# Optimization experiments

Hardware: AMD Instinct MI355X
Metric: run time of the kernel (lower is better)

The kernel has to match this reference:

```python
import jax, jax.numpy as jnp
import numpy as np
import math

NUM_HEADS = 16


def setup_inputs() -> dict:
    key = jax.random.key(0)
    ks = jax.random.split(key, 5)
    L, B, E = 2048, 2, 1024
    scale = 1.0 / math.sqrt(E)
    return {
        "query": jax.random.normal(ks[0], (L, B, E), jnp.float32),
        "key": jax.random.normal(ks[1], (L, B, E), jnp.float32),
        "value": jax.random.normal(ks[2], (L, B, E), jnp.float32),
        "in_proj_weight": jax.random.normal(ks[3], (3 * E, E), jnp.float32) * scale,
        "in_proj_bias": jnp.zeros((3 * E,), jnp.float32),
        "out_w": jax.random.normal(ks[4], (E, E), jnp.float32) * scale,
        "out_b": jnp.zeros((E,), jnp.float32),
    }


def reference(query, key, value, in_proj_weight, in_proj_bias, out_w, out_b):
    L, Bz, E = query.shape
    S = key.shape[0]
    H = NUM_HEADS
    hd = E // H
    # in-projection: chunk packed weight into q/k/v parts (same math as torch chunk)
    w_q, w_k, w_v = jnp.split(in_proj_weight, 3, axis=0)
    b_q, b_k, b_v = jnp.split(in_proj_bias, 3, axis=0)
    q = query @ w_q.T + b_q            # (L, B, E)
    k = key @ w_k.T + b_k              # (S, B, E)
    v = value @ w_v.T + b_v            # (S, B, E)
    # (L, B*H, hd) -> (B*H, L, hd)
    q = q.reshape(L, Bz * H, hd).transpose(1, 0, 2) / math.sqrt(hd)
    k = k.reshape(S, Bz * H, hd).transpose(1, 0, 2)
    v = v.reshape(S, Bz * H, hd).transpose(1, 0, 2)
    # sigmoid attention (non-softmax), full (B*H, L, S) matrix as in original
    attn = jax.nn.sigmoid(jnp.einsum("bld,bsd->bls", q, k))
    denom = attn.sum(axis=-1, keepdims=True) + 1e-4
    out = jnp.einsum("bls,bsd->bld", attn / denom, v)  # (B*H, L, hd)
    out = out.transpose(1, 0, 2).reshape(L, Bz, E)
    out = out @ out_w.T + out_b
    avg_weights = attn.reshape(Bz, H, L, S).sum(axis=1) / H
    return out, avg_weights
```

## Files before the change

### kernel.cpp

```cpp
#include <hip/hip_runtime.h>
#include <stdint.h>


#define L_SEQ 2048
#define NBATCH 2
#define EMB 1024
#define NHEAD 16
#define HD 64
#define MROWS 4096

typedef __bf16 bf16x8 __attribute__((ext_vector_type(8)));
typedef float f32x4 __attribute__((ext_vector_type(4)));

#define WAITVM(N) asm volatile("s_waitcnt vmcnt(" #N ")" ::: "memory")
#define WAITLG() asm volatile("s_waitcnt lgkmcnt(0)" ::: "memory")
#define SBAR()                                  \
  do {                                          \
    asm volatile("" ::: "memory");              \
    __builtin_amdgcn_s_barrier();               \
    asm volatile("" ::: "memory");              \
  } while (0)

#if __has_builtin(__builtin_amdgcn_exp2f)
#define EXP2F(x) __builtin_amdgcn_exp2f(x)
#else
#define EXP2F(x) exp2f(x)
#endif

__device__ __forceinline__ unsigned short f2bf(float f) {
  union { float f; uint32_t u; } v; v.f = f;
  uint32_t u = v.u;
  u += 0x7fffu + ((u >> 16) & 1u);
  return (unsigned short)(u >> 16);
}

__device__ __forceinline__ unsigned short f2bf_fast(float f) {
  union { float f; uint32_t u; } v; v.f = f;
  return (unsigned short)((v.u + 0x8000u) >> 16);
}

__device__ __forceinline__ void gl_lds16(const void* gptr, void* ldsptr) {
  const uint32_t* g = reinterpret_cast<const uint32_t*>(gptr);
  auto* l = reinterpret_cast<__attribute__((address_space(3))) uint32_t*>(
      reinterpret_cast<uintptr_t>(ldsptr));
  __builtin_amdgcn_global_load_lds(g, l, 16, 0, 0);
}

__device__ __forceinline__ f32x4 mfma16(bf16x8 a, bf16x8 b, f32x4 c) {
  return __builtin_amdgcn_mfma_f32_16x16x32_bf16(a, b, c, 0, 0, 0);
}

__device__ __forceinline__ float fast_sigmoid2(float st) {
  float e = EXP2F(st);
  return __builtin_amdgcn_rcpf(1.0f + e);
}

__global__ __launch_bounds__(256) void k_convert(
    const float* __restrict__ qin, const float* __restrict__ kin,
    const float* __restrict__ vin, const float* __restrict__ win,
    const float* __restrict__ wo,
    unsigned short* __restrict__ Xq, unsigned short* __restrict__ Xk,
    unsigned short* __restrict__ Xv, unsigned short* __restrict__ Wb,
    unsigned short* __restrict__ Wob) {
  const int row = blockIdx.x;
  const int t = threadIdx.x;
  const float* src;
  unsigned short* dst;
  int srow;
  size_t drow;
  if (row < 3 * MROWS) {
    const int which = row >> 12;
    const int m = row & (MROWS - 1);
    const int b = m >> 11, l = m & (L_SEQ - 1);
    srow = l * NBATCH + b;
    drow = (size_t)m;
    src = which == 0 ? qin : (which == 1 ? kin : vin);
    dst = which == 0 ? Xq : (which == 1 ? Xk : Xv);
  } else if (row < 3 * MROWS + 3072) {
    srow = row - 3 * MROWS; drow = (size_t)srow; src = win; dst = Wb;
  } else {
    srow = row - (3 * MROWS + 3072); drow = (size_t)srow; src = wo; dst = Wob;
  }
  const float4 vv = *(const float4*)(src + (size_t)srow * EMB + t * 4);
  ushort4 o;
  o.x = f2bf(vv.x); o.y = f2bf(vv.y); o.z = f2bf(vv.z); o.w = f2bf(vv.w);
  *(ushort4*)(dst + drow * EMB + t * 4) = o;
}

__device__ __forceinline__ void gemm_issue(
    const unsigned short* __restrict__ A, const unsigned short* __restrict__ Bm,
    int m0, int n0, int k0, unsigned short* sA, unsigned short* sB) {
  const int tid = threadIdx.x;
  const int wave = tid >> 6;
  const int lane = tid & 63;
  const int srow = lane >> 2;
  const int scol = lane & 3;
  for (int i = 0; i < 2; ++i) {
    const int p = wave * 2 + i;
    const int r = p * 16 + srow;
    const int c = scol ^ ((r >> 1) & 3);
    gl_lds16(A + (size_t)(m0 + r) * EMB + k0 + c * 8, sA + p * 512);
    gl_lds16(Bm + (size_t)(n0 + r) * EMB + k0 + c * 8, sB + p * 512);
  }
}

__device__ __forceinline__ void gemm_core(
    const unsigned short* __restrict__ A, const unsigned short* __restrict__ Bm,
    int m0, int n0, unsigned short* sA, unsigned short* sB, f32x4 acc[4][4]) {
  const int tid = threadIdx.x;
  const int wave = tid >> 6;
  const int lane = tid & 63;
  const int quad = lane >> 4;
  const int l16 = lane & 15;
  const int wm = (wave >> 1) * 64;
  const int wn = (wave & 1) * 64;
  const int NSTEP = EMB / 32;

  for (int mi = 0; mi < 4; ++mi)
    for (int ni = 0; ni < 4; ++ni)
      acc[mi][ni] = (f32x4){0.f, 0.f, 0.f, 0.f};

  gemm_issue(A, Bm, m0, n0, 0, sA, sB);
  gemm_issue(A, Bm, m0, n0, 32, sA + 4096, sB + 4096);

  int cur = 0;
  for (int step = 0; step < NSTEP; ++step) {
    if (step < NSTEP - 1) { WAITVM(4); } else { WAITVM(0); }
    SBAR();
    if (step + 2 < NSTEP) {
      int nxt = cur + 2; if (nxt >= 3) nxt -= 3;
      gemm_issue(A, Bm, m0, n0, (step + 2) * 32, sA + nxt * 4096,
                 sB + nxt * 4096);
    }
    const unsigned short* cA = sA + cur * 4096;
    const unsigned short* cB = sB + cur * 4096;
    bf16x8 af[4], bfr[4];
    for (int mi = 0; mi < 4; ++mi) {
      const int r = wm + mi * 16 + l16;
      const int cp = quad ^ ((r >> 1) & 3);
      af[mi] = *(const bf16x8*)(cA + r * 32 + cp * 8);
    }
    for (int ni = 0; ni < 4; ++ni) {
      const int r = wn + ni * 16 + l16;
      const int cp = quad ^ ((r >> 1) & 3);
      bfr[ni] = *(const bf16x8*)(cB + r * 32 + cp * 8);
    }
    for (int mi = 0; mi < 4; ++mi)
      for (int ni = 0; ni < 4; ++ni)
        acc[mi][ni] = mfma16(af[mi], bfr[ni], acc[mi][ni]);
    cur = cur == 2 ? 0 : cur + 1;
  }
}

__global__ __launch_bounds__(256) void k_inproj(
    const unsigned short* __restrict__ Xq, const unsigned short* __restrict__ Xk,
    const unsigned short* __restrict__ Xv, const unsigned short* __restrict__ Wb,
    const float* __restrict__ bias,
    unsigned short* __restrict__ qb, unsigned short* __restrict__ kb,
    unsigned short* __restrict__ vb) {
  __shared__ __attribute__((aligned(16))) unsigned short sA[3 * 128 * 32];
  __shared__ __attribute__((aligned(16))) unsigned short sB[3 * 128 * 32];
  const int bid = blockIdx.x;
  const int tile = (bid & 7) * 96 + (bid >> 3);
  const int z = tile >> 8;
  const int rem = tile & 255;
  const int m0 = (rem >> 3) * 128;
  const int n0 = (rem & 7) * 128;
  const unsigned short* A = z == 0 ? Xq : (z == 1 ? Xk : Xv);
  f32x4 acc[4][4];
  gemm_core(A, Wb + (size_t)z * EMB * EMB, m0, n0, sA, sB, acc);

  const int tid = threadIdx.x, wave = tid >> 6, lane = tid & 63;
  const int quad = lane >> 4, l16 = lane & 15;
  const int wm = (wave >> 1) * 64, wn = (wave & 1) * 64;
  const float scale = (z == 0) ? -0.18033688011112042f : 1.0f;
  unsigned short* dst01 = (z == 0) ? qb : kb;
  for (int ni = 0; ni < 4; ++ni) {
    const int n = n0 + wn + ni * 16 + l16;
    const float bv = bias[z * EMB + n];
    const int h = n >> 6, d = n & 63;
    for (int mi = 0; mi < 4; ++mi) {
      for (int r = 0; r < 4; ++r) {
        const int m = m0 + wm + mi * 16 + quad * 4 + r;
        const int b = m >> 11, l = m & (L_SEQ - 1);
        const unsigned short o = f2bf((acc[mi][ni][r] + bv) * scale);
        if (z == 2)
          vb[((size_t)(b * NHEAD + h) * HD + d) * L_SEQ + l] = o;
        else
          dst01[((size_t)(b * NHEAD + h) * L_SEQ + l) * HD + d] = o;
      }
    }
  }
}

__global__ __launch_bounds__(512) void k_attn(
    const unsigned short* __restrict__ qb, const unsigned short* __restrict__ kb,
    const unsigned short* __restrict__ vb, unsigned short* __restrict__ oh) {
  __shared__ __attribute__((aligned(16))) unsigned short sK[2][64 * 64];
  __shared__ __attribute__((aligned(16))) unsigned short sV[2][64 * 64];
  __shared__ __attribute__((aligned(16))) unsigned short sP[128 * 72];

  const int bh = blockIdx.x;
  const int b = bh >> 4, h = bh & 15;
  const int l0 = blockIdx.y * 128;
  const unsigned short* qg = qb + ((size_t)bh * L_SEQ + l0) * HD;
  const unsigned short* kg = kb + (size_t)bh * L_SEQ * HD;
  const unsigned short* vg = vb + (size_t)bh * HD * L_SEQ;

  const int tid = threadIdx.x, wave = tid >> 6, lane = tid & 63;
  const int quad = lane >> 4, l16 = lane & 15;
  const int sr8 = lane >> 3, sc8 = lane & 7;
  const int W = wave * 16;

  bf16x8 qf0, qf1;
  {
    const unsigned short* qrow = qg + (size_t)(W + l16) * HD + quad * 8;
    qf0 = *(const bf16x8*)(qrow);
    qf1 = *(const bf16x8*)(qrow + 32);
  }

  if (wave < 4) {
    for (int i = 0; i < 2; ++i) {
      const int p = wave * 2 + i;
      const int r = p * 8 + sr8;
      const int c = sc8 ^ (r & 7);
      gl_lds16(kg + (size_t)r * HD + c * 8, sK[0] + p * 512);
    }
  } else {
    for (int i = 0; i < 2; ++i) {
      const int p = (wave - 4) * 2 + i;
      const int r = p * 8 + sr8;
      const int c = sc8 ^ (r & 7);
      gl_lds16(vg + (size_t)r * L_SEQ + c * 8, sV[0] + p * 512);
    }
  }

  f32x4 oacc[4];
  for (int ni = 0; ni < 4; ++ni) oacc[ni] = (f32x4){0.f, 0.f, 0.f, 0.f};
  f32x4 dacc = (f32x4){0.f, 0.f, 0.f, 0.f};

  bf16x8 ones;
  for (int j = 0; j < 8; ++j) ones[j] = (__bf16)1.0f;

  const int NS = L_SEQ / 64;
  for (int it = 0; it < NS; ++it) {
    const int cur = it & 1;
    WAITVM(0);
    SBAR();
    if (it + 1 < NS) {
      const int s0n = (it + 1) * 64;
      if (wave < 4) {
        for (int i = 0; i < 2; ++i) {
          const int p = wave * 2 + i;
          const int r = p * 8 + sr8;
          const int c = sc8 ^ (r & 7);
          gl_lds16(kg + (size_t)(s0n + r) * HD + c * 8, sK[cur ^ 1] + p * 512);
        }
      } else {
        for (int i = 0; i < 2; ++i) {
          const int p = (wave - 4) * 2 + i;
          const int r = p * 8 + sr8;
          const int c = sc8 ^ (r & 7);
          gl_lds16(vg + (size_t)r * L_SEQ + s0n + c * 8, sV[cur ^ 1] + p * 512);
        }
      }
    }

    f32x4 st[4];
    for (int smi = 0; smi < 4; ++smi) st[smi] = (f32x4){0.f, 0.f, 0.f, 0.f};
    {
      for (int smi = 0; smi < 4; ++smi) {
        const int r = smi * 16 + l16;
        const int c = quad ^ (r & 7);
        bf16x8 a = *(const bf16x8*)(sK[cur] + r * 64 + c * 8);
        st[smi] = mfma16(a, qf0, st[smi]);
      }
    }
    {
      for (int smi = 0; smi < 4; ++smi) {
        const int r = smi * 16 + l16;
        const int c = (4 + quad) ^ (r & 7);
        bf16x8 a = *(const bf16x8*)(sK[cur] + r * 64 + c * 8);
        st[smi] = mfma16(a, qf1, st[smi]);
      }
    }

    for (int smi = 0; smi < 4; ++smi) {
      uint32_t u[4];
      for (int r = 0; r < 4; ++r) {
        union { float f; uint32_t i; } cv;
        cv.f = fast_sigmoid2(st[smi][r]);
        u[r] = cv.i + 0x8000u;
      }
      uint2 pk;
      pk.x = __builtin_amdgcn_perm(u[1], u[0], 0x07060302u);
      pk.y = __builtin_amdgcn_perm(u[3], u[2], 0x07060302u);
      *(uint2*)(sP + (size_t)(W + l16) * 72 + smi * 16 + quad * 4) = pk;
    }
    WAITLG();

    const int lr = W + l16;
    for (int kk = 0; kk < 64; kk += 32) {
      bf16x8 ap = *(const bf16x8*)(sP + (size_t)lr * 72 + kk + quad * 8);
      for (int ni = 0; ni < 4; ++ni) {
        const int rd = ni * 16 + l16;
        const int c = ((kk >> 3) + quad) ^ (rd & 7);
        bf16x8 bv4 = *(const bf16x8*)(sV[cur] + rd * 64 + c * 8);
        oacc[ni] = mfma16(ap, bv4, oacc[ni]);
      }
      dacc = mfma16(ap, ones, dacc);
    }
  }

  for (int r = 0; r < 4; ++r) {
    const int lrow = l0 + wave * 16 + quad * 4 + r;
    const float rden = __builtin_amdgcn_rcpf(dacc[r] + 1e-4f);
    unsigned short* dst = oh + ((size_t)(b * L_SEQ + lrow)) * EMB + h * HD;
    for (int ni = 0; ni < 4; ++ni)
      dst[ni * 16 + l16] = f2bf_fast(oacc[ni][r] * rden);
  }
}

__global__ __launch_bounds__(512) void k_avg(
    const unsigned short* __restrict__ qb, const unsigned short* __restrict__ kb,
    float* __restrict__ avg) {
  __shared__ __attribute__((aligned(16))) unsigned short sQ[2][128 * 64];
  __shared__ __attribute__((aligned(16))) unsigned short sK[2][128 * 64];
  const int ss0 = blockIdx.x * 128, l0 = blockIdx.y * 128, b = blockIdx.z;
  const int tid = threadIdx.x, wave = tid >> 6, lane = tid & 63;
  const int quad = lane >> 4, l16 = lane & 15;
  const int wm = (wave & 1) * 64, wn = (wave >> 1) * 32;
  const int sr8 = lane >> 3, sc8 = lane & 7;

  f32x4 av[4][2];
  for (int mi = 0; mi < 4; ++mi)
    for (int ni = 0; ni < 2; ++ni) av[mi][ni] = (f32x4){0.f, 0.f, 0.f, 0.f};

  auto stage = [&](int hh, int buf) {
    const unsigned short* qg = qb + ((size_t)(b * NHEAD + hh) * L_SEQ + l0) * HD;
    const unsigned short* kg = kb + ((size_t)(b * NHEAD + hh) * L_SEQ + ss0) * HD;
    for (int i = 0; i < 2; ++i) {
      const int p = wave * 2 + i;
      const int r = p * 8 + sr8;
      const int c = sc8 ^ (r & 7);
      gl_lds16(qg + (size_t)r * HD + c * 8, sQ[buf] + p * 512);
      gl_lds16(kg + (size_t)r * HD + c * 8, sK[buf] + p * 512);
    }
  };

  stage(0, 0);

  for (int h = 0; h < NHEAD; ++h) {
    const int cur = h & 1;
    WAITVM(0);
    SBAR();
    if (h + 1 < NHEAD) stage(h + 1, cur ^ 1);

    f32x4 scr[4][2];
    for (int mi = 0; mi < 4; ++mi)
      for (int ni = 0; ni < 2; ++ni) scr[mi][ni] = (f32x4){0.f, 0.f, 0.f, 0.f};
    for (int kk = 0; kk < HD; kk += 32) {
      bf16x8 a[4], bb[2];
      for (int mi = 0; mi < 4; ++mi) {
        const int r = wm + mi * 16 + l16;
        const int c = ((kk >> 3) + quad) ^ (r & 7);
        a[mi] = *(const bf16x8*)(sQ[cur] + r * 64 + c * 8);
      }
      for (int ni = 0; ni < 2; ++ni) {
        const int r = wn + ni * 16 + l16;
        const int c = ((kk >> 3) + quad) ^ (r & 7);
        bb[ni] = *(const bf16x8*)(sK[cur] + r * 64 + c * 8);
      }
      for (int mi = 0; mi < 4; ++mi)
        for (int ni = 0; ni < 2; ++ni)
          scr[mi][ni] = mfma16(a[mi], bb[ni], scr[mi][ni]);
    }
    for (int mi = 0; mi < 4; ++mi)
      for (int ni = 0; ni < 2; ++ni)
        for (int r = 0; r < 4; ++r)
          av[mi][ni][r] += fast_sigmoid2(scr[mi][ni][r]);
  }

  for (int mi = 0; mi < 4; ++mi) {
    for (int r = 0; r < 4; ++r) {
      const int l = l0 + wm + mi * 16 + quad * 4 + r;
      float* dst = avg + ((size_t)b * L_SEQ + l) * L_SEQ + ss0 + wn;
      for (int ni = 0; ni < 2; ++ni)
        dst[ni * 16 + l16] = av[mi][ni][r] * 0.0625f;
    }
  }
}

__global__ __launch_bounds__(256) void k_outproj(
    const unsigned short* __restrict__ OH, const unsigned short* __restrict__ Wob,
    const float* __restrict__ ob, float* __restrict__ out) {
  __shared__ __attribute__((aligned(16))) unsigned short sA[3 * 128 * 32];
  __shared__ __attribute__((aligned(16))) unsigned short sB[3 * 128 * 32];
  const int bid = blockIdx.x;
  const int tile = (bid & 7) * 32 + (bid >> 3);
  const int m0 = (tile >> 3) * 128;
  const int n0 = (tile & 7) * 128;
  f32x4 acc[4][4];
  gemm_core(OH, Wob, m0, n0, sA, sB, acc);

  const int tid = threadIdx.x, wave = tid >> 6, lane = tid & 63;
  const int quad = lane >> 4, l16 = lane & 15;
  const int wm = (wave >> 1) * 64, wn = (wave & 1) * 64;
  for (int ni = 0; ni < 4; ++ni) {
    const int n = n0 + wn + ni * 16 + l16;
    const float bv = ob[n];
    for (int mi = 0; mi < 4; ++mi) {
      for (int r = 0; r < 4; ++r) {
        const int m = m0 + wm + mi * 16 + quad * 4 + r;
        const int b = m >> 11, l = m & (L_SEQ - 1);
        out[((size_t)l * NBATCH + b) * EMB + n] = acc[mi][ni][r] + bv;
      }
    }
  }
}

extern "C" void kernel_launch(void* const* d_in, const int* in_sizes, int n_in,
                              void* d_out, int out_size, void* d_ws, size_t ws_size,
                              hipStream_t stream) {
  (void)in_sizes; (void)n_in; (void)out_size;
  const float* qin = (const float*)d_in[0];
  const float* kin = (const float*)d_in[1];
  const float* vin = (const float*)d_in[2];
  const float* w   = (const float*)d_in[3];
  const float* bias = (const float*)d_in[4];
  const float* wo  = (const float*)d_in[5];
  const float* ob  = (const float*)d_in[6];
  float* out = (float*)d_out;

  unsigned short* Xq  = (unsigned short*)d_ws;
  unsigned short* Xk  = Xq + (size_t)MROWS * EMB;
  unsigned short* Xv  = Xk + (size_t)MROWS * EMB;
  unsigned short* Wb  = Xv + (size_t)MROWS * EMB;
  unsigned short* Wob = Wb + (size_t)3 * EMB * EMB;
  unsigned short* qbuf = Wob + (size_t)EMB * EMB;
  unsigned short* kbuf = qbuf + (size_t)MROWS * EMB;
  unsigned short* vbuf = kbuf + (size_t)MROWS * EMB;
  unsigned short* ohb  = vbuf + (size_t)MROWS * EMB;
  const size_t need = ((size_t)MROWS * EMB * 7 + (size_t)4 * EMB * EMB) * 2;
  if (ws_size < need) return;

  k_convert<<<16384, 256, 0, stream>>>(qin, kin, vin, w, wo, Xq, Xk, Xv, Wb, Wob);
  k_inproj<<<768, 256, 0, stream>>>(Xq, Xk, Xv, Wb, bias, qbuf, kbuf, vbuf);
  k_attn<<<dim3(32, 16), 512, 0, stream>>>(qbuf, kbuf, vbuf, ohb);
  k_avg<<<dim3(16, 16, 2), 512, 0, stream>>>(qbuf, kbuf, out + (size_t)MROWS * EMB);
  k_outproj<<<256, 256, 0, stream>>>(ohb, Wob, ob, out);
}
```

Before: 270.4 us.

## Merge attention and averaged-weights kernels into one launch with shared LDS

Combines the attention kernel and the head-averaged sigmoid weights kernel into a single kernel with 1024 blocks. Block ids below 512 run attention and the rest compute the averaged weights, with both roles using one 64 KB shared buffer. The aim is to let the two independent workloads run on the GPU at the same time and to save one kernel launch and the tail gap between kernels. In exchange, every block reserves the larger LDS footprint, which may limit how many attention blocks fit on a CU, and register use becomes the maximum of the two paths.

```diff
diff --git a/kernel.cpp b/kernel.cpp
--- a/kernel.cpp
+++ b/kernel.cpp
@@ -193,200 +193,206 @@
   }
 }
 
-__global__ __launch_bounds__(512) void k_attn(
+__global__ __launch_bounds__(512) void k_attn_avg(
     const unsigned short* __restrict__ qb, const unsigned short* __restrict__ kb,
-    const unsigned short* __restrict__ vb, unsigned short* __restrict__ oh) {
-  __shared__ __attribute__((aligned(16))) unsigned short sK[2][64 * 64];
-  __shared__ __attribute__((aligned(16))) unsigned short sV[2][64 * 64];
-  __shared__ __attribute__((aligned(16))) unsigned short sP[128 * 72];
-
-  const int bh = blockIdx.x;
-  const int b = bh >> 4, h = bh & 15;
-  const int l0 = blockIdx.y * 128;
-  const unsigned short* qg = qb + ((size_t)bh * L_SEQ + l0) * HD;
-  const unsigned short* kg = kb + (size_t)bh * L_SEQ * HD;
-  const unsigned short* vg = vb + (size_t)bh * HD * L_SEQ;
-
+    const unsigned short* __restrict__ vb, unsigned short* __restrict__ oh,
+    float* __restrict__ avg) {
+  __shared__ __attribute__((aligned(16))) unsigned short smem[32768];
+
+  const int aid = blockIdx.x;
   const int tid = threadIdx.x, wave = tid >> 6, lane = tid & 63;
   const int quad = lane >> 4, l16 = lane & 15;
   const int sr8 = lane >> 3, sc8 = lane & 7;
-  const int W = wave * 16;
-
-  bf16x8 qf0, qf1;
-  {
-    const unsigned short* qrow = qg + (size_t)(W + l16) * HD + quad * 8;
-    qf0 = *(const bf16x8*)(qrow);
-    qf1 = *(const bf16x8*)(qrow + 32);
-  }
-
-  if (wave < 4) {
-    for (int i = 0; i < 2; ++i) {
-      const int p = wave * 2 + i;
-      const int r = p * 8 + sr8;
-      const int c = sc8 ^ (r & 7);
-      gl_lds16(kg + (size_t)r * HD + c * 8, sK[0] + p * 512);
+
+  if (aid < 512) {
+    unsigned short (*sK)[64 * 64] = (unsigned short (*)[64 * 64])(smem);
+    unsigned short (*sV)[64 * 64] = (unsigned short (*)[64 * 64])(smem + 8192);
+    unsigned short* sP = smem + 16384;
+
+    const int bh = aid & 31;
+    const int b = bh >> 4, h = bh & 15;
+    const int l0 = (aid >> 5) * 128;
+    const unsigned short* qg = qb + ((size_t)bh * L_SEQ + l0) * HD;
+    const unsigned short* kg = kb + (size_t)bh * L_SEQ * HD;
+    const unsigned short* vg = vb + (size_t)bh * HD * L_SEQ;
+
+    const int W = wave * 16;
+
+    bf16x8 qf0, qf1;
+    {
+      const unsigned short* qrow = qg + (size_t)(W + l16) * HD + quad * 8;
+      qf0 = *(const bf16x8*)(qrow);
+      qf1 = *(const bf16x8*)(qrow + 32);
+    }
+
+    if (wave < 4) {
+      for (int i = 0; i < 2; ++i) {
+        const int p = wave * 2 + i;
+        const int r = p * 8 + sr8;
+        const int c = sc8 ^ (r & 7);
+        gl_lds16(kg + (size_t)r * HD + c * 8, sK[0] + p * 512);
+      }
+    } else {
+      for (int i = 0; i < 2; ++i) {
+        const int p = (wave - 4) * 2 + i;
+        const int r = p * 8 + sr8;
+        const int c = sc8 ^ (r & 7);
+        gl_lds16(vg + (size_t)r * L_SEQ + c * 8, sV[0] + p * 512);
+      }
+    }
+
+    f32x4 oacc[4];
+    for (int ni = 0; ni < 4; ++ni) oacc[ni] = (f32x4){0.f, 0.f, 0.f, 0.f};
+    f32x4 dacc = (f32x4){0.f, 0.f, 0.f, 0.f};
+
+    bf16x8 ones;
+    for (int j = 0; j < 8; ++j) ones[j] = (__bf16)1.0f;
+
+    const int NS = L_SEQ / 64;
+    for (int it = 0; it < NS; ++it) {
+      const int cur = it & 1;
+      WAITVM(0);
+      SBAR();
+      if (it + 1 < NS) {
+        const int s0n = (it + 1) * 64;
+        if (wave < 4) {
+          for (int i = 0; i < 2; ++i) {
+            const int p = wave * 2 + i;
+            const int r = p * 8 + sr8;
+            const int c = sc8 ^ (r & 7);
+            gl_lds16(kg + (size_t)(s0n + r) * HD + c * 8, sK[cur ^ 1] + p * 512);
+          }
+        } else {
+          for (int i = 0; i < 2; ++i) {
+            const int p = (wave - 4) * 2 + i;
+            const int r = p * 8 + sr8;
+            const int c = sc8 ^ (r & 7);
+            gl_lds16(vg + (size_t)r * L_SEQ + s0n + c * 8, sV[cur ^ 1] + p * 512);
+          }
+        }
+      }
+
+      f32x4 st[4];
+      for (int smi = 0; smi < 4; ++smi) st[smi] = (f32x4){0.f, 0.f, 0.f, 0.f};
+      {
+        for (int smi = 0; smi < 4; ++smi) {
+          const int r = smi * 16 + l16;
+          const int c = quad ^ (r & 7);
+          bf16x8 a = *(const bf16x8*)(sK[cur] + r * 64 + c * 8);
+          st[smi] = mfma16(a, qf0, st[smi]);
+        }
+      }
+      {
+        for (int smi = 0; smi < 4; ++smi) {
+          const int r = smi * 16 + l16;
+          const int c = (4 + quad) ^ (r & 7);
+          bf16x8 a = *(const bf16x8*)(sK[cur] + r * 64 + c * 8);
+          st[smi] = mfma16(a, qf1, st[smi]);
+        }
+      }
+
+      for (int smi = 0; smi < 4; ++smi) {
+        uint32_t u[4];
+        for (int r = 0; r < 4; ++r) {
+          union { float f; uint32_t i; } cv;
+          cv.f = fast_sigmoid2(st[smi][r]);
+          u[r] = cv.i + 0x8000u;
+        }
+        uint2 pk;
+        pk.x = __builtin_amdgcn_perm(u[1], u[0], 0x07060302u);
+        pk.y = __builtin_amdgcn_perm(u[3], u[2], 0x07060302u);
+        *(uint2*)(sP + (size_t)(W + l16) * 72 + smi * 16 + quad * 4) = pk;
+      }
+      WAITLG();
+
+      const int lr = W + l16;
+      for (int kk = 0; kk < 64; kk += 32) {
+        bf16x8 ap = *(const bf16x8*)(sP + (size_t)lr * 72 + kk + quad * 8);
+        for (int ni = 0; ni < 4; ++ni) {
+          const int rd = ni * 16 + l16;
+          const int c = ((kk >> 3) + quad) ^ (rd & 7);
+          bf16x8 bv4 = *(const bf16x8*)(sV[cur] + rd * 64 + c * 8);
+          oacc[ni] = mfma16(ap, bv4, oacc[ni]);
+        }
+        dacc = mfma16(ap, ones, dacc);
+      }
+    }
+
+    for (int r = 0; r < 4; ++r) {
+      const int lrow = l0 + wave * 16 + quad * 4 + r;
+      const float rden = __builtin_amdgcn_rcpf(dacc[r] + 1e-4f);
+      unsigned short* dst = oh + ((size_t)(b * L_SEQ + lrow)) * EMB + h * HD;
+      for (int ni = 0; ni < 4; ++ni)
+        dst[ni * 16 + l16] = f2bf_fast(oacc[ni][r] * rden);
     }
   } else {
-    for (int i = 0; i < 2; ++i) {
-      const int p = (wave - 4) * 2 + i;
-      const int r = p * 8 + sr8;
-      const int c = sc8 ^ (r & 7);
-      gl_lds16(vg + (size_t)r * L_SEQ + c * 8, sV[0] + p * 512);
-    }
-  }
-
-  f32x4 oacc[4];
-  for (int ni = 0; ni < 4; ++ni) oacc[ni] = (f32x4){0.f, 0.f, 0.f, 0.f};
-  f32x4 dacc = (f32x4){0.f, 0.f, 0.f, 0.f};
-
-  bf16x8 ones;
-  for (int j = 0; j < 8; ++j) ones[j] = (__bf16)1.0f;
-
-  const int NS = L_SEQ / 64;
-  for (int it = 0; it < NS; ++it) {
-    const int cur = it & 1;
-    WAITVM(0);
-    SBAR();
-    if (it + 1 < NS) {
-      const int s0n = (it + 1) * 64;
-      if (wave < 4) {
-        for (int i = 0; i < 2; ++i) {
-          const int p = wave * 2 + i;
-          const int r = p * 8 + sr8;
-          const int c = sc8 ^ (r & 7);
-          gl_lds16(kg + (size_t)(s0n + r) * HD + c * 8, sK[cur ^ 1] + p * 512);
-        }
-      } else {
-        for (int i = 0; i < 2; ++i) {
-          const int p = (wave - 4) * 2 + i;
-          const int r = p * 8 + sr8;
-          const int c = sc8 ^ (r & 7);
-          gl_lds16(vg + (size_t)r * L_SEQ + s0n + c * 8, sV[cur ^ 1] + p * 512);
-        }
-      }
-    }
-
-    f32x4 st[4];
-    for (int smi = 0; smi < 4; ++smi) st[smi] = (f32x4){0.f, 0.f, 0.f, 0.f};
-    {
-      for (int smi = 0; smi < 4; ++smi) {
-        const int r = smi * 16 + l16;
-        const int c = quad ^ (r & 7);
-        bf16x8 a = *(const bf16x8*)(sK[cur] + r * 64 + c * 8);
-        st[smi] = mfma16(a, qf0, st[smi]);
-      }
-    }
-    {
-      for (int smi = 0; smi < 4; ++smi) {
-        const int r = smi * 16 + l16;
-        const int c = (4 + quad) ^ (r & 7);
-        bf16x8 a = *(const bf16x8*)(sK[cur] + r * 64 + c * 8);
-        st[smi] = mfma16(a, qf1, st[smi]);
-      }
-    }
-
-    for (int smi = 0; smi < 4; ++smi) {
-      uint32_t u[4];
-      for (int r = 0; r < 4; ++r) {
-        union { float f; uint32_t i; } cv;
-        cv.f = fast_sigmoid2(st[smi][r]);
-        u[r] = cv.i + 0x8000u;
-      }
-      uint2 pk;
-      pk.x = __builtin_amdgcn_perm(u[1], u[0], 0x07060302u);
-      pk.y = __builtin_amdgcn_perm(u[3], u[2], 0x07060302u);
-      *(uint2*)(sP + (size_t)(W + l16) * 72 + smi * 16 + quad * 4) = pk;
-    }
-    WAITLG();
-
-    const int lr = W + l16;
-    for (int kk = 0; kk < 64; kk += 32) {
-      bf16x8 ap = *(const bf16x8*)(sP + (size_t)lr * 72 + kk + quad * 8);
-      for (int ni = 0; ni < 4; ++ni) {
-        const int rd = ni * 16 + l16;
-        const int c = ((kk >> 3) + quad) ^ (rd & 7);
-        bf16x8 bv4 = *(const bf16x8*)(sV[cur] + rd * 64 + c * 8);
-        oacc[ni] = mfma16(ap, bv4, oacc[ni]);
-      }
-      dacc = mfma16(ap, ones, dacc);
-    }
-  }
-
-  for (int r = 0; r < 4; ++r) {
-    const int lrow = l0 + wave * 16 + quad * 4 + r;
-    const float rden = __builtin_amdgcn_rcpf(dacc[r] + 1e-4f);
-    unsigned short* dst = oh + ((size_t)(b * L_SEQ + lrow)) * EMB + h * HD;
-    for (int ni = 0; ni < 4; ++ni)
-      dst[ni * 16 + l16] = f2bf_fast(oacc[ni][r] * rden);
-  }
-}
-
-__global__ __launch_bounds__(512) void k_avg(
-    const unsigned short* __restrict__ qb, const unsigned short* __restrict__ kb,
-    float* __restrict__ avg) {
-  __shared__ __attribute__((aligned(16))) unsigned short sQ[2][128 * 64];
-  __shared__ __attribute__((aligned(16))) unsigned short sK[2][128 * 64];
-  const int ss0 = blockIdx.x * 128, l0 = blockIdx.y * 128, b = blockIdx.z;
-  const int tid = threadIdx.x, wave = tid >> 6, lane = tid & 63;
-  const int quad = lane >> 4, l16 = lane & 15;
-  const int wm = (wave & 1) * 64, wn = (wave >> 1) * 32;
-  const int sr8 = lane >> 3, sc8 = lane & 7;
-
-  f32x4 av[4][2];
-  for (int mi = 0; mi < 4; ++mi)
-    for (int ni = 0; ni < 2; ++ni) av[mi][ni] = (f32x4){0.f, 0.f, 0.f, 0.f};
-
-  auto stage = [&](int hh, int buf) {
-    const unsigned short* qg = qb + ((size_t)(b * NHEAD + hh) * L_SEQ + l0) * HD;
-    const unsigned short* kg = kb + ((size_t)(b * NHEAD + hh) * L_SEQ + ss0) * HD;
-    for (int i = 0; i < 2; ++i) {
-      const int p = wave * 2 + i;
-      const int r = p * 8 + sr8;
-      const int c = sc8 ^ (r & 7);
-      gl_lds16(qg + (size_t)r * HD + c * 8, sQ[buf] + p * 512);
-      gl_lds16(kg + (size_t)r * HD + c * 8, sK[buf] + p * 512);
-    }
-  };
-
-  stage(0, 0);
-
-  for (int h = 0; h < NHEAD; ++h) {
-    const int cur = h & 1;
-    WAITVM(0);
-    SBAR();
-    if (h + 1 < NHEAD) stage(h + 1, cur ^ 1);
-
-    f32x4 scr[4][2];
+    unsigned short (*sQ)[128 * 64] = (unsigned short (*)[128 * 64])(smem);
+    unsigned short (*sK)[128 * 64] = (unsigned short (*)[128 * 64])(smem + 16384);
+
+    const int avgid = aid - 512;
+    const int ss0 = (avgid & 15) * 128;
+    const int l0 = ((avgid >> 4) & 15) * 128;
+    const int b = avgid >> 8;
+    const int wm = (wave & 1) * 64, wn = (wave >> 1) * 32;
+
+    f32x4 av[4][2];
     for (int mi = 0; mi < 4; ++mi)
-      for (int ni = 0; ni < 2; ++ni) scr[mi][ni] = (f32x4){0.f, 0.f, 0.f, 0.f};
-    for (int kk = 0; kk < HD; kk += 32) {
-      bf16x8 a[4], bb[2];
-      for (int mi = 0; mi < 4; ++mi) {
-        const int r = wm + mi * 16 + l16;
-        const int c = ((kk >> 3) + quad) ^ (r & 7);
-        a[mi] = *(const bf16x8*)(sQ[cur] + r * 64 + c * 8);
-      }
-      for (int ni = 0; ni < 2; ++ni) {
-        const int r = wn + ni * 16 + l16;
-        const int c = ((kk >> 3) + quad) ^ (r & 7);
-        bb[ni] = *(const bf16x8*)(sK[cur] + r * 64 + c * 8);
+      for (int ni = 0; ni < 2; ++ni) av[mi][ni] = (f32x4){0.f, 0.f, 0.f, 0.f};
+
+    auto stage = [&](int hh, int buf) {
+      const unsigned short* qg =
+          qb + ((size_t)(b * NHEAD + hh) * L_SEQ + l0) * HD;
+      const unsigned short* kg =
+          kb + ((size_t)(b * NHEAD + hh) * L_SEQ + ss0) * HD;
+      for (int i = 0; i < 2; ++i) {
+        const int p = wave * 2 + i;
+        const int r = p * 8 + sr8;
+        const int c = sc8 ^ (r & 7);
+        gl_lds16(qg + (size_t)r * HD + c * 8, sQ[buf] + p * 512);
+        gl_lds16(kg + (size_t)r * HD + c * 8, sK[buf] + p * 512);
+      }
+    };
+
+    stage(0, 0);
+
+    for (int h = 0; h < NHEAD; ++h) {
+      const int cur = h & 1;
+      WAITVM(0);
+      SBAR();
+      if (h + 1 < NHEAD) stage(h + 1, cur ^ 1);
+
+      f32x4 scr[4][2];
+      for (int mi = 0; mi < 4; ++mi)
+        for (int ni = 0; ni < 2; ++ni) scr[mi][ni] = (f32x4){0.f, 0.f, 0.f, 0.f};
+      for (int kk = 0; kk < HD; kk += 32) {
+        bf16x8 a[4], bbv[2];
+        for (int mi = 0; mi < 4; ++mi) {
+          const int r = wm + mi * 16 + l16;
+          const int c = ((kk >> 3) + quad) ^ (r & 7);
+          a[mi] = *(const bf16x8*)(sQ[cur] + r * 64 + c * 8);
+        }
+        for (int ni = 0; ni < 2; ++ni) {
+          const int r = wn + ni * 16 + l16;
+          const int c = ((kk >> 3) + quad) ^ (r & 7);
+          bbv[ni] = *(const bf16x8*)(sK[cur] + r * 64 + c * 8);
+        }
+        for (int mi = 0; mi < 4; ++mi)
+          for (int ni = 0; ni < 2; ++ni)
+            scr[mi][ni] = mfma16(a[mi], bbv[ni], scr[mi][ni]);
       }
       for (int mi = 0; mi < 4; ++mi)
         for (int ni = 0; ni < 2; ++ni)
-          scr[mi][ni] = mfma16(a[mi], bb[ni], scr[mi][ni]);
-    }
-    for (int mi = 0; mi < 4; ++mi)
-      for (int ni = 0; ni < 2; ++ni)
-        for (int r = 0; r < 4; ++r)
-          av[mi][ni][r] += fast_sigmoid2(scr[mi][ni][r]);
-  }
-
-  for (int mi = 0; mi < 4; ++mi) {
-    for (int r = 0; r < 4; ++r) {
-      const int l = l0 + wm + mi * 16 + quad * 4 + r;
-      float* dst = avg + ((size_t)b * L_SEQ + l) * L_SEQ + ss0 + wn;
-      for (int ni = 0; ni < 2; ++ni)
-        dst[ni * 16 + l16] = av[mi][ni][r] * 0.0625f;
+          for (int r = 0; r < 4; ++r)
+            av[mi][ni][r] += fast_sigmoid2(scr[mi][ni][r]);
+    }
+
+    for (int mi = 0; mi < 4; ++mi) {
+      for (int r = 0; r < 4; ++r) {
+        const int l = l0 + wm + mi * 16 + quad * 4 + r;
+        float* dst = avg + ((size_t)b * L_SEQ + l) * L_SEQ + ss0 + wn;
+        for (int ni = 0; ni < 2; ++ni)
+          dst[ni * 16 + l16] = av[mi][ni][r] * 0.0625f;
+      }
     }
   }
 }
@@ -446,7 +452,7 @@
 
   k_convert<<<16384, 256, 0, stream>>>(qin, kin, vin, w, wo, Xq, Xk, Xv, Wb, Wob);
   k_inproj<<<768, 256, 0, stream>>>(Xq, Xk, Xv, Wb, bias, qbuf, kbuf, vbuf);
-  k_attn<<<dim3(32, 16), 512, 0, stream>>>(qbuf, kbuf, vbuf, ohb);
-  k_avg<<<dim3(16, 16, 2), 512, 0, stream>>>(qbuf, kbuf, out + (size_t)MROWS * EMB);
+  k_attn_avg<<<1024, 512, 0, stream>>>(qbuf, kbuf, vbuf, ohb,
+                                       out + (size_t)MROWS * EMB);
   k_outproj<<<256, 256, 0, stream>>>(ohb, Wob, ob, out);
 }
```

Result: faster. 256.7 us (-5.1%).
